# Kernel tuning notes

Measured on AMD Instinct MI355X. Metric: run time of the kernel, lower is better.

The kernel has to match this reference:

```python
import jax, jax.numpy as jnp
import numpy as np

N = 100000   # nodes
E = 3200000  # edges
NC = 32


def cheb_conv(x, row, col, W, b):
    """PyG ChebConv with sym normalization and default lambda_max=2.
    Scaled Laplacian L_hat = 2L/lambda_max - I has zero diagonal and
    off-diagonal weights -d_i^{-1/2} d_j^{-1/2} (self-loops removed first).
    W: [K, in, out], b: [out] or None.
    """
    n = x.shape[0]
    ew = jnp.where(row != col, 1.0, 0.0).astype(x.dtype)  # remove_self_loops
    deg = jax.ops.segment_sum(ew, row, num_segments=n)
    dinv = jnp.where(deg > 0, jax.lax.rsqrt(jnp.maximum(deg, 1e-12)), 0.0)
    w = -ew * dinv[row] * dinv[col]  # [E] edge weights of L_hat

    def L(v):  # L_hat @ v via gather + segment-sum scatter
        return jax.ops.segment_sum(w[:, None] * v[col], row, num_segments=n)

    K = W.shape[0]
    Tx0 = x
    out = Tx0 @ W[0]
    if K > 1:
        Tx1 = L(x)
        out = out + Tx1 @ W[1]
        for k in range(2, K):  # Chebyshev recurrence T_k = 2 L T_{k-1} - T_{k-2}
            Tx2 = 2.0 * L(Tx1) - Tx0
            out = out + Tx2 @ W[k]
            Tx0, Tx1 = Tx1, Tx2
    if b is not None:
        out = out + b
    return out


def setup_inputs() -> dict:
    key = jax.random.key(0)
    ks = jax.random.split(key, 10)
    x = jax.random.normal(ks[0], (N, 3), dtype=jnp.float32)
    edge_index = jax.random.randint(ks[1], (2, E), 0, N, dtype=jnp.int64)
    batch = jnp.zeros((N,), dtype=jnp.int64)
    edge_attr = jax.random.normal(ks[2], (E, 1), dtype=jnp.float32)
    s = 0.1
    W1 = jax.random.normal(ks[3], (24, 3, NC), dtype=jnp.float32) * s
    b1 = jnp.zeros((NC,), dtype=jnp.float32)
    W2 = jax.random.normal(ks[4], (12, NC, NC), dtype=jnp.float32) * s
    b2 = jnp.zeros((NC,), dtype=jnp.float32)
    W3 = jax.random.normal(ks[5], (10, NC, NC), dtype=jnp.float32) * s
    b3 = jnp.zeros((NC,), dtype=jnp.float32)
    W4 = jax.random.normal(ks[6], (1, NC, 1), dtype=jnp.float32) * s
    return {"x": x, "edge_index": edge_index, "batch": batch, "edge_attr": edge_attr,
            "W1": W1, "b1": b1, "W2": W2, "b2": b2, "W3": W3, "b3": b3, "W4": W4}


def reference(x, edge_index, batch, edge_attr, W1, b1, W2, b2, W3, b3, W4):
    # batch and edge_attr are unused by ChebNet.forward (kept for signature parity)
    row, col = edge_index[0], edge_index[1]
    h = jax.nn.silu(cheb_conv(x, row, col, W1, b1))
    h = jax.nn.silu(cheb_conv(h, row, col, W2, b2))
    h = jax.nn.silu(cheb_conv(h, row, col, W3, b3))
    return cheb_conv(h, row, col, W4, None)  # block4: K=1, bias=False
```

## Files before the change

### kernel.cpp

```cpp
#include <hip/hip_runtime.h>
#include <math.h>

#define NN 100000
#define EE 3200000
#define NCH 32
#define CAP 96
#define FILL_PASSES 8
#define HB 3200256

typedef unsigned short ushortT;
typedef unsigned int uintT;

__device__ __forceinline__ ushortT f2b(float f) {
  uintT u = __float_as_uint(f);
  uintT r = u + 0x7fffu + ((u >> 16) & 1u);
  return (ushortT)(r >> 16);
}
__device__ __forceinline__ uintT pack2(float x, float y) {
  return (uintT)f2b(x) | ((uintT)f2b(y) << 16);
}
__device__ __forceinline__ float lo2f(uintT u) { return __uint_as_float(u << 16); }
__device__ __forceinline__ float hi2f(uintT u) { return __uint_as_float(u & 0xffff0000u); }
__device__ __forceinline__ float silu(float v) { return v / (1.f + expf(-v)); }


__global__ void init_cursor_k(int* __restrict__ cur) {
  int i = blockIdx.x * blockDim.x + threadIdx.x;
  if (i < NN) cur[i] = i * CAP;
}

__global__ void fill_k(const int* __restrict__ ei, int* __restrict__ cursor,
                       int* __restrict__ colc, int lo, int hi) {
  int t = blockIdx.x * blockDim.x + threadIdx.x;
  if (t * 4 >= EE) return;
  int4 r4 = ((const int4*)ei)[t];
  bool i0 = r4.x >= lo && r4.x < hi;
  bool i1 = r4.y >= lo && r4.y < hi;
  bool i2 = r4.z >= lo && r4.z < hi;
  bool i3 = r4.w >= lo && r4.w < hi;
  if (!(i0 | i1 | i2 | i3)) return;
  int4 c4 = ((const int4*)(ei + EE))[t];
  if (i0 && r4.x != c4.x) colc[atomicAdd(&cursor[r4.x], 1)] = c4.x;
  if (i1 && r4.y != c4.y) colc[atomicAdd(&cursor[r4.y], 1)] = c4.y;
  if (i2 && r4.z != c4.z) colc[atomicAdd(&cursor[r4.z], 1)] = c4.z;
  if (i3 && r4.w != c4.w) colc[atomicAdd(&cursor[r4.w], 1)] = c4.w;
}

__global__ void dinv_k(const int* __restrict__ rend, float* __restrict__ dinv,
                       float* __restrict__ d2, float* __restrict__ sqd) {
  int i = blockIdx.x * blockDim.x + threadIdx.x;
  if (i >= NN) return;
  int c = rend[i] - i * CAP;
  float di = (c > 0) ? rsqrtf((float)c) : 0.f;
  dinv[i] = di;
  d2[i] = di * di;
  sqd[i] = (c > 0) ? sqrtf((float)c) : 1.f;
}

__global__ void sent_f3_k(uint2* __restrict__ Vfb) {
  int t = threadIdx.x;
  if (t < 24) Vfb[(size_t)t * (NN + 1) + NN] = make_uint2(0u, 0u);
}

__global__ void sent_b16_k(uintT* __restrict__ Vh0, uintT* __restrict__ Vh1,
                           char* __restrict__ R) {
  int t = threadIdx.x;
  int tb = t >> 3, d = t & 7;
  if (tb >= 14) return;
  uintT* base;
  if (tb == 12) base = Vh0;
  else if (tb == 13) base = Vh1;
  else base = (uintT*)(R + (size_t)tb * HB);
  base[(size_t)NN * 8 + d] = 0u;
}

__global__ __launch_bounds__(256) void prescale_x_k(const float* __restrict__ x,
                                                    const float* __restrict__ dinv,
                                                    uint2* __restrict__ V0) {
  int i = blockIdx.x * blockDim.x + threadIdx.x;
  if (i >= NN) return;
  float di = dinv[i];
  V0[i] = make_uint2(pack2(di * x[3 * i], di * x[3 * i + 1]),
                     pack2(di * x[3 * i + 2], 0.f));
}


template <bool FIRST>
__global__ __launch_bounds__(256) void cheb_f3_k(
    const int* __restrict__ rend, const int* __restrict__ colc,
    const float* __restrict__ d2, const uint2* __restrict__ U,
    const uint2* __restrict__ A, uint2* __restrict__ Vo) {
  int t8 = blockIdx.x * blockDim.x + threadIdx.x;
  int i = t8 >> 3, q = t8 & 7;
  if (i >= NN) return;
  int s = i * CAP, e = rend[i];
  float a0 = 0.f, a1 = 0.f, a2 = 0.f;
  for (int t = s + q; t < e; t += 32) {
#pragma unroll
    for (int u = 0; u < 4; ++u) {
      int tt = t + 8 * u;
      int cc = (tt < e) ? colc[tt] : NN;
      uint2 r = U[cc];
      a0 += lo2f(r.x); a1 += hi2f(r.x); a2 += lo2f(r.y);
    }
  }
  a0 += __shfl_xor(a0, 1); a1 += __shfl_xor(a1, 1); a2 += __shfl_xor(a2, 1);
  a0 += __shfl_xor(a0, 2); a1 += __shfl_xor(a1, 2); a2 += __shfl_xor(a2, 2);
  a0 += __shfl_xor(a0, 4); a1 += __shfl_xor(a1, 4); a2 += __shfl_xor(a2, 4);
  if (q == 0) {
    float d2i = d2[i];
    float v0, v1, v2;
    if (FIRST) {
      v0 = -d2i * a0; v1 = -d2i * a1; v2 = -d2i * a2;
    } else {
      uint2 ap = A[i];
      v0 = fmaf(-2.f * d2i, a0, -lo2f(ap.x));
      v1 = fmaf(-2.f * d2i, a1, -hi2f(ap.x));
      v2 = fmaf(-2.f * d2i, a2, -lo2f(ap.y));
    }
    Vo[i] = make_uint2(pack2(v0, v1), pack2(v2, 0.f));
  }
}

template <int K0, int K1>
__device__ __forceinline__ void sum_planes(const uint2* __restrict__ Vfb, int i,
                                           const float* __restrict__ W1,
                                           float* __restrict__ s_) {
#pragma unroll
  for (int k = K0; k < K1; ++k) {
    uint2 u = Vfb[(size_t)k * (NN + 1) + i];
    float v0 = lo2f(u.x), v1 = hi2f(u.x), v2 = lo2f(u.y);
    const float* Wk = W1 + k * 96;
#pragma unroll
    for (int j = 0; j < 32; ++j)
      s_[j] = fmaf(v0, Wk[j], fmaf(v1, Wk[32 + j], fmaf(v2, Wk[64 + j], s_[j])));
  }
}

__global__ __launch_bounds__(256) void gemm_l1_k(
    const float* __restrict__ x, const uint2* __restrict__ Vfb,
    const float* __restrict__ W1, const float* __restrict__ b1,
    const float* __restrict__ dinv, const float* __restrict__ sqd,
    ushortT* __restrict__ Vh0, ushortT* __restrict__ Vh1) {
  __shared__ float red[4 * 64 * 36];
  int tid = threadIdx.x;
  int w = tid >> 6, lane = tid & 63;
  int i = blockIdx.x * 64 + lane;
  float s_[32];
#pragma unroll
  for (int j = 0; j < 32; ++j) s_[j] = 0.f;
  if (i < NN) {
    if (w == 0) sum_planes<1, 7>(Vfb, i, W1, s_);
    else if (w == 1) sum_planes<7, 13>(Vfb, i, W1, s_);
    else if (w == 2) sum_planes<13, 19>(Vfb, i, W1, s_);
    else sum_planes<19, 24>(Vfb, i, W1, s_);
  }
  float* rb = &red[(w * 64 + lane) * 36];
#pragma unroll
  for (int j = 0; j < 32; ++j) rb[j] = s_[j];
  __syncthreads();
  int r = tid >> 2, q = tid & 3;
  int io = blockIdx.x * 64 + r;
  if (io >= NN) return;
  float acc8[8];
#pragma unroll
  for (int c = 0; c < 8; ++c) acc8[c] = 0.f;
#pragma unroll
  for (int ww = 0; ww < 4; ++ww) {
    const float* p = &red[(ww * 64 + r) * 36 + q * 8];
#pragma unroll
    for (int c = 0; c < 8; ++c) acc8[c] += p[c];
  }
  float x0 = x[3 * io], x1 = x[3 * io + 1], x2 = x[3 * io + 2];
  float sq = sqd[io], di = dinv[io];
  uintT o[4];
#pragma unroll
  for (int cp = 0; cp < 4; ++cp) {
    int j0 = q * 8 + 2 * cp, j1 = j0 + 1;
    float g0 = fmaf(sq, acc8[2 * cp],
        fmaf(x0, W1[j0], fmaf(x1, W1[32 + j0], fmaf(x2, W1[64 + j0], b1[j0]))));
    float g1 = fmaf(sq, acc8[2 * cp + 1],
        fmaf(x0, W1[j1], fmaf(x1, W1[32 + j1], fmaf(x2, W1[64 + j1], b1[j1]))));
    o[cp] = pack2(di * silu(g0), di * silu(g1));
  }
  uintT* dst = (uintT*)((q >> 1) ? Vh1 : Vh0) + (size_t)io * 8 + (q & 1) * 4;
  *(uint4*)dst = make_uint4(o[0], o[1], o[2], o[3]);
}


template <bool FIRST>
__global__ __launch_bounds__(256) void cheb_bh_k(
    const int* __restrict__ rend, const int* __restrict__ colc,
    const float* __restrict__ d2, const uintT* __restrict__ U,
    const uintT* __restrict__ Ap, uintT* __restrict__ Vo) {
  int t = blockIdx.x * blockDim.x + threadIdx.x;
  int i = t >> 3;
  if (i >= NN) return;
  int g = t & 7;
  int lb = (threadIdx.x & 63) & 56;
  int s = i * CAP, e = rend[i];
  float ax = 0.f, ay = 0.f;
  for (int b = s; b < e; b += 8) {
    int idx = b + g;
    int cl = (idx < e) ? colc[idx] : NN;
#pragma unroll
    for (int u = 0; u < 8; ++u) {
      int cj = __shfl(cl, lb + u);
      uintT r = U[(size_t)cj * 8 + g];
      ax += lo2f(r); ay += hi2f(r);
    }
  }
  float d2i = d2[i];
  float vx, vy;
  if (FIRST) {
    vx = -d2i * ax; vy = -d2i * ay;
  } else {
    uintT au = Ap[(size_t)i * 8 + g];
    vx = fmaf(-2.f * d2i, ax, -lo2f(au));
    vy = fmaf(-2.f * d2i, ay, -hi2f(au));
  }
  Vo[(size_t)i * 8 + g] = pack2(vx, vy);
}

__device__ __forceinline__ void fma_pair(uintT dw, const float* __restrict__ Wc,
                                         float a[32]) {
  float vl = lo2f(dw), vh = hi2f(dw);
#pragma unroll
  for (int j = 0; j < 32; ++j) a[j] = fmaf(vl, Wc[j], a[j]);
#pragma unroll
  for (int j = 0; j < 32; ++j) a[j] = fmaf(vh, Wc[32 + j], a[j]);
}

__device__ __forceinline__ void plane_fma(const uintT* __restrict__ h0,
                                          const uintT* __restrict__ h1, size_t i,
                                          const float* __restrict__ W, float a[32]) {
  uint4 u0 = *(const uint4*)(h0 + i * 8);
  uint4 u1 = *(const uint4*)(h0 + i * 8 + 4);
  uint4 u2 = *(const uint4*)(h1 + i * 8);
  uint4 u3 = *(const uint4*)(h1 + i * 8 + 4);
  fma_pair(u0.x, W + 0 * 64, a);   fma_pair(u0.y, W + 1 * 64, a);
  fma_pair(u0.z, W + 2 * 64, a);   fma_pair(u0.w, W + 3 * 64, a);
  fma_pair(u1.x, W + 4 * 64, a);   fma_pair(u1.y, W + 5 * 64, a);
  fma_pair(u1.z, W + 6 * 64, a);   fma_pair(u1.w, W + 7 * 64, a);
  fma_pair(u2.x, W + 8 * 64, a);   fma_pair(u2.y, W + 9 * 64, a);
  fma_pair(u2.z, W + 10 * 64, a);  fma_pair(u2.w, W + 11 * 64, a);
  fma_pair(u3.x, W + 12 * 64, a);  fma_pair(u3.y, W + 13 * 64, a);
  fma_pair(u3.z, W + 14 * 64, a);  fma_pair(u3.w, W + 15 * 64, a);
}

template <int NP, bool INIT>
__global__ __launch_bounds__(256) void gemm_ch_k(
    const uintT* __restrict__ A0, const uintT* __restrict__ A1,
    const uintT* __restrict__ B0, const uintT* __restrict__ B1,
    const float* __restrict__ W, float* __restrict__ acc) {
  int i = blockIdx.x * blockDim.x + threadIdx.x;
  if (i >= NN) return;
  float a[32];
  float4* ar = (float4*)(acc + (size_t)i * 32);
  if (INIT) {
#pragma unroll
    for (int j = 0; j < 32; ++j) a[j] = 0.f;
  } else {
#pragma unroll
    for (int q = 0; q < 8; ++q) {
      float4 v = ar[q];
      a[4 * q] = v.x; a[4 * q + 1] = v.y; a[4 * q + 2] = v.z; a[4 * q + 3] = v.w;
    }
  }
  plane_fma(A0, A1, (size_t)i, W, a);
  if (NP == 2) plane_fma(B0, B1, (size_t)i, W + 1024, a);
#pragma unroll
  for (int q = 0; q < 8; ++q)
    ar[q] = make_float4(a[4 * q], a[4 * q + 1], a[4 * q + 2], a[4 * q + 3]);
}

__global__ __launch_bounds__(256) void silu2_k(const float* __restrict__ acc,
                                               const float* __restrict__ b,
                                               const float* __restrict__ sqd,
                                               const float* __restrict__ dinv,
                                               ushortT* __restrict__ Vh0,
                                               ushortT* __restrict__ Vh1) {
  int t = blockIdx.x * blockDim.x + threadIdx.x;
  if (t >= NN * NCH) return;
  int i = t >> 5, j = t & 31;
  float g = fmaf(sqd[i], acc[t], b[j]);
  ushortT uv = f2b(dinv[i] * silu(g));
  if (j < 16) Vh0[(size_t)i * 16 + j] = uv;
  else        Vh1[(size_t)i * 16 + (j - 16)] = uv;
}

__global__ __launch_bounds__(256) void final2_k(const float* __restrict__ acc,
                                                const float* __restrict__ b3,
                                                const float* __restrict__ sqd,
                                                const float* __restrict__ W4,
                                                float* __restrict__ out) {
  int i = blockIdx.x * blockDim.x + threadIdx.x;
  if (i >= NN) return;
  const float4* ar = (const float4*)(acc + (size_t)i * 32);
  float sq = sqd[i];
  float g = 0.f;
#pragma unroll
  for (int q = 0; q < 8; ++q) {
    float4 v = ar[q];
    g = fmaf(silu(fmaf(sq, v.x, b3[4 * q + 0])), W4[4 * q + 0], g);
    g = fmaf(silu(fmaf(sq, v.y, b3[4 * q + 1])), W4[4 * q + 1], g);
    g = fmaf(silu(fmaf(sq, v.z, b3[4 * q + 2])), W4[4 * q + 2], g);
    g = fmaf(silu(fmaf(sq, v.w, b3[4 * q + 3])), W4[4 * q + 3], g);
  }
  out[i] = g;
}


extern "C" void kernel_launch(void* const* d_in, const int* in_sizes, int n_in,
                              void* d_out, int out_size, void* d_ws, size_t ws_size,
                              hipStream_t stream) {
  const float* x = (const float*)d_in[0];
  const int* ei = (const int*)d_in[1];
  const float* W1 = (const float*)d_in[4];
  const float* b1 = (const float*)d_in[5];
  const float* W2 = (const float*)d_in[6];
  const float* b2 = (const float*)d_in[7];
  const float* W3 = (const float*)d_in[8];
  const float* b3 = (const float*)d_in[9];
  const float* W4 = (const float*)d_in[10];
  float* out = (float*)d_out;

  char* ws = (char*)d_ws;
  size_t off = 0;
  auto alloc = [&](size_t bytes) {
    void* p = ws + off;
    off += (bytes + 255) & ~(size_t)255;
    return p;
  };
  int* rend = (int*)alloc((size_t)NN * 4);
  float* dinv = (float*)alloc((size_t)NN * 4);
  float* d2 = (float*)alloc((size_t)NN * 4);
  float* sqd = (float*)alloc((size_t)NN * 4);
  int* colc = (int*)alloc((size_t)NN * CAP * 4);
  ushortT* Vh0 = (ushortT*)alloc(HB);
  ushortT* Vh1 = (ushortT*)alloc(HB);
  float* acc = (float*)alloc((size_t)NN * NCH * 4);
  char* R = (char*)alloc((size_t)12 * HB);
  uint2* Vfb = (uint2*)R;
  (void)ws_size; (void)in_sizes; (void)n_in; (void)out_size;

  const int GR = (NN + 255) / 256;
  const int GE = (NN * NCH + 255) / 256;
  const int GR8 = (NN * 8 + 255) / 256;
  const int GL1 = (NN + 63) / 64;

  init_cursor_k<<<GR, 256, 0, stream>>>(rend);
  {
    int step = (NN + FILL_PASSES - 1) / FILL_PASSES;
    for (int p = 0; p < FILL_PASSES; ++p) {
      int lo = p * step;
      int hi = (lo + step < NN) ? lo + step : NN;
      fill_k<<<(EE / 4 + 255) / 256, 256, 0, stream>>>(ei, rend, colc, lo, hi);
    }
  }
  dinv_k<<<GR, 256, 0, stream>>>(rend, dinv, d2, sqd);

  sent_f3_k<<<1, 64, 0, stream>>>(Vfb);
  prescale_x_k<<<GR, 256, 0, stream>>>(x, dinv, Vfb);
  auto Vp = [&](int k) { return Vfb + (size_t)k * (NN + 1); };
  cheb_f3_k<true><<<GR8, 256, 0, stream>>>(rend, colc, d2, Vp(0), nullptr, Vp(1));
  for (int k = 2; k < 24; ++k)
    cheb_f3_k<false><<<GR8, 256, 0, stream>>>(rend, colc, d2, Vp(k - 1), Vp(k - 2), Vp(k));
  gemm_l1_k<<<GL1, 256, 0, stream>>>(x, Vfb, W1, b1, dinv, sqd, Vh0, Vh1);

  sent_b16_k<<<1, 128, 0, stream>>>((uintT*)Vh0, (uintT*)Vh1, R);
  auto ringH = [&](int k, int h) {
    return (uintT*)(R + (size_t)(((k - 1) % 6) * 2 + h) * HB);
  };
  auto run_layer = [&](const float* W, int K) {
    gemm_ch_k<1, true><<<GR, 256, 0, stream>>>((uintT*)Vh0, (uintT*)Vh1,
                                               nullptr, nullptr, W, acc);
    for (int k = 1; k < K; ++k) {
      for (int h = 0; h < 2; ++h) {
        const uintT* U = (k == 1) ? (h ? (uintT*)Vh1 : (uintT*)Vh0) : ringH(k - 1, h);
        if (k == 1)
          cheb_bh_k<true><<<GR8, 256, 0, stream>>>(rend, colc, d2, U, nullptr,
                                                   ringH(k, h));
        else {
          const uintT* Ap = (k == 2) ? (h ? (uintT*)Vh1 : (uintT*)Vh0) : ringH(k - 2, h);
          cheb_bh_k<false><<<GR8, 256, 0, stream>>>(rend, colc, d2, U, Ap,
                                                    ringH(k, h));
        }
      }
      if ((k & 1) == 0)
        gemm_ch_k<2, false><<<GR, 256, 0, stream>>>(
            ringH(k - 1, 0), ringH(k - 1, 1), ringH(k, 0), ringH(k, 1),
            W + (size_t)(k - 1) * 1024, acc);
    }
    if ((K - 1) & 1)
      gemm_ch_k<1, false><<<GR, 256, 0, stream>>>(
          ringH(K - 1, 0), ringH(K - 1, 1), nullptr, nullptr,
          W + (size_t)(K - 1) * 1024, acc);
  };
  run_layer(W2, 12);
  silu2_k<<<GE, 256, 0, stream>>>(acc, b2, sqd, dinv, Vh0, Vh1);
  run_layer(W3, 10);
  final2_k<<<GR, 256, 0, stream>>>(acc, b3, sqd, W4, out);
}
```

Before: 1.870 ms.

## Fuse half-plane Chebyshev propagation, batch GEMM planes, merge prep kernels

The two per-half cheb_bh_k launches are merged into one cheb_bf_k kernel. Each of the 8 lanes per node now gathers a uint2 of 4 bf16 channels, so neighbor indices are read and shuffled once per node instead of once per half. The per-channel accumulation GEMM now consumes up to 4 Chebyshev planes per pass instead of 2, which cuts read-modify-write traffic on the fp32 accumulator and the number of launches. The degree, sentinel and prescale kernels are folded into a single prep kernel. In exchange, each lane holds more accumulator registers and the ring-buffer plane scheduling becomes more intricate.

```diff
diff --git a/kernel.cpp b/kernel.cpp
--- a/kernel.cpp
+++ b/kernel.cpp
@@ -46,8 +46,12 @@
   if (i3 && r4.w != c4.w) colc[atomicAdd(&cursor[r4.w], 1)] = c4.w;
 }
 
-__global__ void dinv_k(const int* __restrict__ rend, float* __restrict__ dinv,
-                       float* __restrict__ d2, float* __restrict__ sqd) {
+__global__ __launch_bounds__(256) void prep_k(
+    const int* __restrict__ rend, const float* __restrict__ x,
+    float* __restrict__ dinv, float* __restrict__ d2, float* __restrict__ sqd,
+    uint2* __restrict__ Vfb) {
+  if (blockIdx.x == 0 && threadIdx.x < 24)
+    Vfb[(size_t)threadIdx.x * (NN + 1) + NN] = make_uint2(0u, 0u);
   int i = blockIdx.x * blockDim.x + threadIdx.x;
   if (i >= NN) return;
   int c = rend[i] - i * CAP;
@@ -55,11 +59,8 @@
   dinv[i] = di;
   d2[i] = di * di;
   sqd[i] = (c > 0) ? sqrtf((float)c) : 1.f;
-}
-
-__global__ void sent_f3_k(uint2* __restrict__ Vfb) {
-  int t = threadIdx.x;
-  if (t < 24) Vfb[(size_t)t * (NN + 1) + NN] = make_uint2(0u, 0u);
+  Vfb[i] = make_uint2(pack2(di * x[3 * i], di * x[3 * i + 1]),
+                      pack2(di * x[3 * i + 2], 0.f));
 }
 
 __global__ void sent_b16_k(uintT* __restrict__ Vh0, uintT* __restrict__ Vh1,
@@ -72,16 +73,6 @@
   else if (tb == 13) base = Vh1;
   else base = (uintT*)(R + (size_t)tb * HB);
   base[(size_t)NN * 8 + d] = 0u;
-}
-
-__global__ __launch_bounds__(256) void prescale_x_k(const float* __restrict__ x,
-                                                    const float* __restrict__ dinv,
-                                                    uint2* __restrict__ V0) {
-  int i = blockIdx.x * blockDim.x + threadIdx.x;
-  if (i >= NN) return;
-  float di = dinv[i];
-  V0[i] = make_uint2(pack2(di * x[3 * i], di * x[3 * i + 1]),
-                     pack2(di * x[3 * i + 2], 0.f));
 }
 
 
@@ -189,37 +180,45 @@
 
 
 template <bool FIRST>
-__global__ __launch_bounds__(256) void cheb_bh_k(
+__global__ __launch_bounds__(256) void cheb_bf_k(
     const int* __restrict__ rend, const int* __restrict__ colc,
-    const float* __restrict__ d2, const uintT* __restrict__ U,
-    const uintT* __restrict__ Ap, uintT* __restrict__ Vo) {
+    const float* __restrict__ d2,
+    const uint2* __restrict__ U0, const uint2* __restrict__ U1,
+    const uint2* __restrict__ A0, const uint2* __restrict__ A1,
+    uint2* __restrict__ V0, uint2* __restrict__ V1) {
   int t = blockIdx.x * blockDim.x + threadIdx.x;
   int i = t >> 3;
   if (i >= NN) return;
   int g = t & 7;
   int lb = (threadIdx.x & 63) & 56;
+  const uint2* T = (g < 4) ? U0 : U1;
+  int c2 = g & 3;
   int s = i * CAP, e = rend[i];
-  float ax = 0.f, ay = 0.f;
+  float a0 = 0.f, a1 = 0.f, a2 = 0.f, a3 = 0.f;
   for (int b = s; b < e; b += 8) {
     int idx = b + g;
     int cl = (idx < e) ? colc[idx] : NN;
 #pragma unroll
     for (int u = 0; u < 8; ++u) {
       int cj = __shfl(cl, lb + u);
-      uintT r = U[(size_t)cj * 8 + g];
-      ax += lo2f(r); ay += hi2f(r);
+      uint2 r = T[(size_t)cj * 4 + c2];
+      a0 += lo2f(r.x); a1 += hi2f(r.x);
+      a2 += lo2f(r.y); a3 += hi2f(r.y);
     }
   }
   float d2i = d2[i];
-  float vx, vy;
+  float v0, v1, v2, v3;
   if (FIRST) {
-    vx = -d2i * ax; vy = -d2i * ay;
+    v0 = -d2i * a0; v1 = -d2i * a1; v2 = -d2i * a2; v3 = -d2i * a3;
   } else {
-    uintT au = Ap[(size_t)i * 8 + g];
-    vx = fmaf(-2.f * d2i, ax, -lo2f(au));
-    vy = fmaf(-2.f * d2i, ay, -hi2f(au));
-  }
-  Vo[(size_t)i * 8 + g] = pack2(vx, vy);
+    uint2 au = ((g < 4) ? A0 : A1)[(size_t)i * 4 + c2];
+    v0 = fmaf(-2.f * d2i, a0, -lo2f(au.x));
+    v1 = fmaf(-2.f * d2i, a1, -hi2f(au.x));
+    v2 = fmaf(-2.f * d2i, a2, -lo2f(au.y));
+    v3 = fmaf(-2.f * d2i, a3, -hi2f(au.y));
+  }
+  ((g < 4) ? V0 : V1)[(size_t)i * 4 + c2] =
+      make_uint2(pack2(v0, v1), pack2(v2, v3));
 }
 
 __device__ __forceinline__ void fma_pair(uintT dw, const float* __restrict__ Wc,
@@ -252,6 +251,8 @@
 __global__ __launch_bounds__(256) void gemm_ch_k(
     const uintT* __restrict__ A0, const uintT* __restrict__ A1,
     const uintT* __restrict__ B0, const uintT* __restrict__ B1,
+    const uintT* __restrict__ C0, const uintT* __restrict__ C1,
+    const uintT* __restrict__ D0, const uintT* __restrict__ D1,
     const float* __restrict__ W, float* __restrict__ acc) {
   int i = blockIdx.x * blockDim.x + threadIdx.x;
   if (i >= NN) return;
@@ -268,7 +269,9 @@
     }
   }
   plane_fma(A0, A1, (size_t)i, W, a);
-  if (NP == 2) plane_fma(B0, B1, (size_t)i, W + 1024, a);
+  if (NP >= 2) plane_fma(B0, B1, (size_t)i, W + 1024, a);
+  if (NP >= 3) plane_fma(C0, C1, (size_t)i, W + 2048, a);
+  if (NP >= 4) plane_fma(D0, D1, (size_t)i, W + 3072, a);
 #pragma unroll
   for (int q = 0; q < 8; ++q)
     ar[q] = make_float4(a[4 * q], a[4 * q + 1], a[4 * q + 2], a[4 * q + 3]);
@@ -358,10 +361,8 @@
       fill_k<<<(EE / 4 + 255) / 256, 256, 0, stream>>>(ei, rend, colc, lo, hi);
     }
   }
-  dinv_k<<<GR, 256, 0, stream>>>(rend, dinv, d2, sqd);
-
-  sent_f3_k<<<1, 64, 0, stream>>>(Vfb);
-  prescale_x_k<<<GR, 256, 0, stream>>>(x, dinv, Vfb);
+  prep_k<<<GR, 256, 0, stream>>>(rend, x, dinv, d2, sqd, Vfb);
+
   auto Vp = [&](int k) { return Vfb + (size_t)k * (NN + 1); };
   cheb_f3_k<true><<<GR8, 256, 0, stream>>>(rend, colc, d2, Vp(0), nullptr, Vp(1));
   for (int k = 2; k < 24; ++k)
@@ -369,33 +370,39 @@
   gemm_l1_k<<<GL1, 256, 0, stream>>>(x, Vfb, W1, b1, dinv, sqd, Vh0, Vh1);
 
   sent_b16_k<<<1, 128, 0, stream>>>((uintT*)Vh0, (uintT*)Vh1, R);
-  auto ringH = [&](int k, int h) {
+  auto Rh = [&](int k, int h) {
     return (uintT*)(R + (size_t)(((k - 1) % 6) * 2 + h) * HB);
   };
   auto run_layer = [&](const float* W, int K) {
-    gemm_ch_k<1, true><<<GR, 256, 0, stream>>>((uintT*)Vh0, (uintT*)Vh1,
-                                               nullptr, nullptr, W, acc);
     for (int k = 1; k < K; ++k) {
-      for (int h = 0; h < 2; ++h) {
-        const uintT* U = (k == 1) ? (h ? (uintT*)Vh1 : (uintT*)Vh0) : ringH(k - 1, h);
-        if (k == 1)
-          cheb_bh_k<true><<<GR8, 256, 0, stream>>>(rend, colc, d2, U, nullptr,
-                                                   ringH(k, h));
-        else {
-          const uintT* Ap = (k == 2) ? (h ? (uintT*)Vh1 : (uintT*)Vh0) : ringH(k - 2, h);
-          cheb_bh_k<false><<<GR8, 256, 0, stream>>>(rend, colc, d2, U, Ap,
-                                                    ringH(k, h));
-        }
+      const uint2* U0 = (k == 1) ? (const uint2*)Vh0 : (const uint2*)Rh(k - 1, 0);
+      const uint2* U1 = (k == 1) ? (const uint2*)Vh1 : (const uint2*)Rh(k - 1, 1);
+      if (k == 1) {
+        cheb_bf_k<true><<<GR8, 256, 0, stream>>>(
+            rend, colc, d2, U0, U1, nullptr, nullptr,
+            (uint2*)Rh(k, 0), (uint2*)Rh(k, 1));
+      } else {
+        const uint2* A0 = (k == 2) ? (const uint2*)Vh0 : (const uint2*)Rh(k - 2, 0);
+        const uint2* A1 = (k == 2) ? (const uint2*)Vh1 : (const uint2*)Rh(k - 2, 1);
+        cheb_bf_k<false><<<GR8, 256, 0, stream>>>(
+            rend, colc, d2, U0, U1, A0, A1, (uint2*)Rh(k, 0), (uint2*)Rh(k, 1));
       }
-      if ((k & 1) == 0)
-        gemm_ch_k<2, false><<<GR, 256, 0, stream>>>(
-            ringH(k - 1, 0), ringH(k - 1, 1), ringH(k, 0), ringH(k, 1),
-            W + (size_t)(k - 1) * 1024, acc);
-    }
-    if ((K - 1) & 1)
-      gemm_ch_k<1, false><<<GR, 256, 0, stream>>>(
-          ringH(K - 1, 0), ringH(K - 1, 1), nullptr, nullptr,
-          W + (size_t)(K - 1) * 1024, acc);
+      if (k == 3) {
+        gemm_ch_k<4, true><<<GR, 256, 0, stream>>>(
+            (uintT*)Vh0, (uintT*)Vh1, Rh(1, 0), Rh(1, 1), Rh(2, 0), Rh(2, 1),
+            Rh(3, 0), Rh(3, 1), W, acc);
+      } else if (k > 3 && (k % 3) == 0) {
+        gemm_ch_k<3, false><<<GR, 256, 0, stream>>>(
+            Rh(k - 2, 0), Rh(k - 2, 1), Rh(k - 1, 0), Rh(k - 1, 1),
+            Rh(k, 0), Rh(k, 1), nullptr, nullptr, W + (size_t)(k - 2) * 1024, acc);
+      }
+    }
+    int last = K - 1;
+    if (last % 3 == 2) {
+      gemm_ch_k<2, false><<<GR, 256, 0, stream>>>(
+          Rh(last - 1, 0), Rh(last - 1, 1), Rh(last, 0), Rh(last, 1),
+          nullptr, nullptr, nullptr, nullptr, W + (size_t)(last - 1) * 1024, acc);
+    }
   };
   run_layer(W2, 12);
   silu2_k<<<GE, 256, 0, stream>>>(acc, b2, sqd, dinv, Vh0, Vh1);
```

After: 2.056 ms. +9.9%, slower.
